# Kernel optimization log

Measured on AMD Instinct MI355X. Metric: run time of the kernel, lower is better.

## Reference

```python
import jax, jax.numpy as jnp
import numpy as np

N_NODES = 100000
N_EDGES = 800000
C = 128  # in_channels_0


def setup_inputs() -> dict:
    key = jax.random.key(0)
    k1, k2, k3, k4 = jax.random.split(key, 4)
    x_0 = jax.random.normal(k1, (N_NODES, C), dtype=jnp.float32)
    source = jax.random.randint(k2, (N_EDGES,), 0, N_NODES, dtype=jnp.int64)
    target = jax.random.randint(k3, (N_EDGES,), 0, N_NODES, dtype=jnp.int64)
    # att: (2C, 1), xavier-uniform-like scale
    limit = float(np.sqrt(6.0 / (2 * C + 1)) * np.sqrt(2.0))
    att = jax.random.uniform(k4, (2 * C, 1), dtype=jnp.float32, minval=-limit, maxval=limit)
    return {"x_0": x_0, "source": source, "target": target, "att": att}


def reference(x_0, source, target, att):
    # edge_signal = relu(concat(x_0[source], x_0[target]) @ att)
    # Split att to avoid materializing the concatenated (E, 2C) tensor:
    # concat(a, b) @ [w1; w2] == a @ w1 + b @ w2 (same math, fewer bytes).
    w_src = att[:C]   # (C, 1)
    w_tgt = att[C:]   # (C, 1)
    edge_signal = x_0[source] @ w_src + x_0[target] @ w_tgt  # (E, 1)
    return jax.nn.relu(edge_signal)
```

## Files before the change

kernel.cpp:

```cpp
#include <hip/hip_runtime.h>

__global__ __launch_bounds__(256) void node_dots_kernel(
    const float* __restrict__ x, const float* __restrict__ att,
    float* __restrict__ s, float* __restrict__ t, int n_pairs) {
  int gtid = blockIdx.x * blockDim.x + threadIdx.x;
  int pair = gtid >> 6;
  int lane = threadIdx.x & 63;
  if (pair >= n_pairs) return;

  const float4* xr = (const float4*)x + (size_t)pair * 64 + lane;
  float4 v = *xr;

  int wl = lane & 31;
  const float4* a4 = (const float4*)att;
  float4 ws = a4[wl];
  float4 wt = a4[32 + wl];

  float ps = v.x * ws.x + v.y * ws.y + v.z * ws.z + v.w * ws.w;
  float pt = v.x * wt.x + v.y * wt.y + v.z * wt.z + v.w * wt.w;

  #pragma unroll
  for (int off = 16; off; off >>= 1) {
    ps += __shfl_down(ps, off);
    pt += __shfl_down(pt, off);
  }
  if (wl == 0) {
    int n = 2 * pair + (lane >> 5);
    s[n] = ps;
    t[n] = pt;
  }
}

__global__ __launch_bounds__(256) void edge_signal_kernel(
    const int* __restrict__ src, const int* __restrict__ tgt,
    const float* __restrict__ s, const float* __restrict__ t,
    float* __restrict__ out, int n_edges) {
  int i = blockIdx.x * blockDim.x + threadIdx.x;
  if (i >= n_edges) return;
  float v = s[src[i]] + t[tgt[i]];
  out[i] = v > 0.0f ? v : 0.0f;
}

extern "C" void kernel_launch(void* const* d_in, const int* in_sizes, int n_in,
                              void* d_out, int out_size, void* d_ws, size_t ws_size,
                              hipStream_t stream) {
  const float* x_0  = (const float*)d_in[0];
  const int*   src  = (const int*)d_in[1];
  const int*   tgt  = (const int*)d_in[2];
  const float* att  = (const float*)d_in[3];
  float* out = (float*)d_out;

  const int C = 128;
  int n_nodes = in_sizes[0] / C;
  int n_edges = in_sizes[1];

  float* s = (float*)d_ws;
  float* t = s + n_nodes;

  int n_pairs = (n_nodes + 1) / 2;
  int waves_per_block = 256 / 64;
  int grid1 = (n_pairs + waves_per_block - 1) / waves_per_block;
  node_dots_kernel<<<grid1, 256, 0, stream>>>(x_0, att, s, t, n_pairs);

  int grid2 = (n_edges + 255) / 256;
  edge_signal_kernel<<<grid2, 256, 0, stream>>>(src, tgt, s, t, out, n_edges);
}
```

Baseline: 99.85 us.

## Use grid-stride 4-way unrolled node dots and vectorized 4-edge gather kernel

After: 101.6 us. Within noise of the previous version (+1.8%).

```diff
diff --git a/kernel.cpp b/kernel.cpp
--- a/kernel.cpp
+++ b/kernel.cpp
@@ -1,33 +1,60 @@
 #include <hip/hip_runtime.h>
 
-__global__ __launch_bounds__(256) void node_dots_kernel(
-    const float* __restrict__ x, const float* __restrict__ att,
-    float* __restrict__ s, float* __restrict__ t, int n_pairs) {
-  int gtid = blockIdx.x * blockDim.x + threadIdx.x;
-  int pair = gtid >> 6;
-  int lane = threadIdx.x & 63;
-  if (pair >= n_pairs) return;
 
-  const float4* xr = (const float4*)x + (size_t)pair * 64 + lane;
-  float4 v = *xr;
+__device__ __forceinline__ float dot4(float4 a, float4 b) {
+  return a.x * b.x + a.y * b.y + a.z * b.z + a.w * b.w;
+}
 
-  int wl = lane & 31;
-  const float4* a4 = (const float4*)att;
-  float4 ws = a4[wl];
-  float4 wt = a4[32 + wl];
-
-  float ps = v.x * ws.x + v.y * ws.y + v.z * ws.z + v.w * ws.w;
-  float pt = v.x * wt.x + v.y * wt.y + v.z * wt.z + v.w * wt.w;
-
+__device__ __forceinline__ void reduce_store(float ps, float pt, int pair, int lane,
+                                             float* __restrict__ s,
+                                             float* __restrict__ t) {
   #pragma unroll
   for (int off = 16; off; off >>= 1) {
     ps += __shfl_down(ps, off);
     pt += __shfl_down(pt, off);
   }
-  if (wl == 0) {
+  if ((lane & 31) == 0) {
     int n = 2 * pair + (lane >> 5);
     s[n] = ps;
     t[n] = pt;
+  }
+}
+
+__global__ __launch_bounds__(256) void node_dots_kernel(
+    const float* __restrict__ x, const float* __restrict__ att,
+    float* __restrict__ s, float* __restrict__ t, int n_pairs) {
+  const int lane = threadIdx.x & 63;
+  const int wave = (blockIdx.x * blockDim.x + threadIdx.x) >> 6;
+  const int n_waves = (gridDim.x * blockDim.x) >> 6;
+  const int wl = lane & 31;
+
+  const float4* a4 = (const float4*)att;
+  const float4 ws = a4[wl];
+  const float4 wt = a4[32 + wl];
+  const float4* xb = (const float4*)x;
+
+  int i = wave;
+  for (; i + 3 * n_waves < n_pairs; i += 4 * n_waves) {
+    const int i0 = i;
+    const int i1 = i + n_waves;
+    const int i2 = i + 2 * n_waves;
+    const int i3 = i + 3 * n_waves;
+    float4 v0 = xb[(size_t)i0 * 64 + lane];
+    float4 v1 = xb[(size_t)i1 * 64 + lane];
+    float4 v2 = xb[(size_t)i2 * 64 + lane];
+    float4 v3 = xb[(size_t)i3 * 64 + lane];
+    float ps0 = dot4(v0, ws), pt0 = dot4(v0, wt);
+    float ps1 = dot4(v1, ws), pt1 = dot4(v1, wt);
+    float ps2 = dot4(v2, ws), pt2 = dot4(v2, wt);
+    float ps3 = dot4(v3, ws), pt3 = dot4(v3, wt);
+    reduce_store(ps0, pt0, i0, lane, s, t);
+    reduce_store(ps1, pt1, i1, lane, s, t);
+    reduce_store(ps2, pt2, i2, lane, s, t);
+    reduce_store(ps3, pt3, i3, lane, s, t);
+  }
+  for (; i < n_pairs; i += n_waves) {
+    float4 v = xb[(size_t)i * 64 + lane];
+    reduce_store(dot4(v, ws), dot4(v, wt), i, lane, s, t);
   }
 }
 
@@ -35,19 +62,36 @@
     const int* __restrict__ src, const int* __restrict__ tgt,
     const float* __restrict__ s, const float* __restrict__ t,
     float* __restrict__ out, int n_edges) {
-  int i = blockIdx.x * blockDim.x + threadIdx.x;
-  if (i >= n_edges) return;
-  float v = s[src[i]] + t[tgt[i]];
-  out[i] = v > 0.0f ? v : 0.0f;
+  int q = blockIdx.x * blockDim.x + threadIdx.x;
+  int n_quads = n_edges >> 2;
+  if (q < n_quads) {
+    int4 sv = ((const int4*)src)[q];
+    int4 tv = ((const int4*)tgt)[q];
+    float a = s[sv.x] + t[tv.x];
+    float b = s[sv.y] + t[tv.y];
+    float c = s[sv.z] + t[tv.z];
+    float d = s[sv.w] + t[tv.w];
+    float4 r;
+    r.x = fmaxf(a, 0.0f);
+    r.y = fmaxf(b, 0.0f);
+    r.z = fmaxf(c, 0.0f);
+    r.w = fmaxf(d, 0.0f);
+    ((float4*)out)[q] = r;
+  } else if (q == n_quads) {
+    for (int e = n_quads * 4; e < n_edges; ++e) {
+      float v = s[src[e]] + t[tgt[e]];
+      out[e] = fmaxf(v, 0.0f);
+    }
+  }
 }
 
 extern "C" void kernel_launch(void* const* d_in, const int* in_sizes, int n_in,
                               void* d_out, int out_size, void* d_ws, size_t ws_size,
                               hipStream_t stream) {
-  const float* x_0  = (const float*)d_in[0];
-  const int*   src  = (const int*)d_in[1];
-  const int*   tgt  = (const int*)d_in[2];
-  const float* att  = (const float*)d_in[3];
+  const float* x_0 = (const float*)d_in[0];
+  const int*   src = (const int*)d_in[1];
+  const int*   tgt = (const int*)d_in[2];
+  const float* att = (const float*)d_in[3];
   float* out = (float*)d_out;
 
   const int C = 128;
@@ -58,10 +102,14 @@
   float* t = s + n_nodes;
 
   int n_pairs = (n_nodes + 1) / 2;
-  int waves_per_block = 256 / 64;
-  int grid1 = (n_pairs + waves_per_block - 1) / waves_per_block;
+  int grid1 = 1024;
+  int max_grid1 = (n_pairs + 3) / 4;
+  if (grid1 > max_grid1) grid1 = max_grid1;
   node_dots_kernel<<<grid1, 256, 0, stream>>>(x_0, att, s, t, n_pairs);
 
-  int grid2 = (n_edges + 255) / 256;
+  int n_quads = n_edges >> 2;
+  int work2 = n_quads + ((n_edges & 3) ? 1 : 0);
+  if (work2 == 0) work2 = 1;
+  int grid2 = (work2 + 255) / 256;
   edge_signal_kernel<<<grid2, 256, 0, stream>>>(src, tgt, s, t, out, n_edges);
 }
```
